# Optimization experiments

Hardware: AMD Instinct MI355X
Metric: run time of the kernel (lower is better)

## Reference

```python
import jax, jax.numpy as jnp
import numpy as np

N = 16384


def setup_inputs() -> dict:
    key = jax.random.key(0)
    k1, k2 = jax.random.split(key)
    logits = jax.random.normal(k1, (N,), dtype=jnp.float32)
    targets = jax.random.randint(k2, (N,), 0, 2, dtype=jnp.int64)
    return {"logits": logits, "targets": targets}


def reference(logits, targets):
    # sigmoid scores for every sample
    s = jax.nn.sigmoid(logits)  # [N]
    pos = (targets != 0).astype(s.dtype)  # [N] mask of positives
    neg = (targets == 0).astype(s.dtype)  # [N] mask of negatives
    # all-pairs pos-vs-neg surrogate: (1 - (s_pos - s_neg))^2
    d = 1.0 - (s[:, None] - s[None, :])  # [N, N]
    loss = jnp.sum((pos[:, None] * neg[None, :]) * (d * d))
    n_pos = jnp.sum(pos)
    n_neg = jnp.sum(neg)
    return loss / (n_pos * n_neg)
```

## Files before the change

### kernel.cpp

```cpp
#include <hip/hip_runtime.h>


#define BLOCK 1024

__global__ __launch_bounds__(BLOCK) void auc_stats_kernel(
    const float* __restrict__ logits, const int* __restrict__ targets,
    float* __restrict__ out, int n) {
  const int tid = threadIdx.x;

  float acc[6] = {0.f, 0.f, 0.f, 0.f, 0.f, 0.f};

  const int n4 = n >> 2;
  const float4* l4 = reinterpret_cast<const float4*>(logits);
  const int4*   t4 = reinterpret_cast<const int4*>(targets);

  for (int i = tid; i < n4; i += BLOCK) {
    float4 lv = l4[i];
    int4   tv = t4[i];
    float xs[4] = {lv.x, lv.y, lv.z, lv.w};
    int   ts[4] = {tv.x, tv.y, tv.z, tv.w};
#pragma unroll
    for (int k = 0; k < 4; ++k) {
      float s  = 1.0f / (1.0f + __expf(-xs[k]));
      float s2 = s * s;
      float p  = (ts[k] != 0) ? 1.0f : 0.0f;
      float q  = 1.0f - p;
      acc[0] += p;       acc[1] += q;
      acc[2] += p * s;   acc[3] += q * s;
      acc[4] += p * s2;  acc[5] += q * s2;
    }
  }
  for (int i = (n4 << 2) + tid; i < n; i += BLOCK) {
    float s  = 1.0f / (1.0f + __expf(-logits[i]));
    float s2 = s * s;
    float p  = (targets[i] != 0) ? 1.0f : 0.0f;
    float q  = 1.0f - p;
    acc[0] += p;       acc[1] += q;
    acc[2] += p * s;   acc[3] += q * s;
    acc[4] += p * s2;  acc[5] += q * s2;
  }

#pragma unroll
  for (int j = 0; j < 6; ++j) {
#pragma unroll
    for (int m = 1; m < 64; m <<= 1) {
      acc[j] += __shfl_xor(acc[j], m, 64);
    }
  }

  __shared__ float lds[BLOCK / 64][6];
  const int wave = tid >> 6;
  const int lane = tid & 63;
  if (lane == 0) {
#pragma unroll
    for (int j = 0; j < 6; ++j) lds[wave][j] = acc[j];
  }
  __syncthreads();

  if (tid == 0) {
    double t[6] = {0, 0, 0, 0, 0, 0};
    for (int w = 0; w < BLOCK / 64; ++w)
      for (int j = 0; j < 6; ++j) t[j] += (double)lds[w][j];

    double np_ = t[0], nn = t[1], sp = t[2], sn = t[3], sp2 = t[4], sn2 = t[5];
    double loss = np_ * nn
                - 2.0 * nn * sp
                + 2.0 * np_ * sn
                + nn * sp2
                + np_ * sn2
                - 2.0 * sp * sn;
    out[0] = (float)(loss / (np_ * nn));
  }
}

extern "C" void kernel_launch(void* const* d_in, const int* in_sizes, int n_in,
                              void* d_out, int out_size, void* d_ws, size_t ws_size,
                              hipStream_t stream) {
  const float* logits  = (const float*)d_in[0];
  const int*   targets = (const int*)d_in[1];
  float*       out     = (float*)d_out;
  const int n = in_sizes[0];

  auc_stats_kernel<<<dim3(1), dim3(BLOCK), 0, stream>>>(logits, targets, out, n);
}
```

Baseline: 10.77 us.

## Split reduction across 64 single-wave blocks with a second combine kernel

Replaces the single 1024-thread block with 64 blocks of one wave each, which write per-block partial sums to workspace. A second one-wave kernel reduces those partials in double and computes the final loss. This spreads the memory reads across many CUs instead of one, at the cost of an extra kernel launch and a global round trip.

```diff
diff --git a/kernel.cpp b/kernel.cpp
--- a/kernel.cpp
+++ b/kernel.cpp
@@ -1,12 +1,14 @@
 #include <hip/hip_runtime.h>
 
 
-#define BLOCK 1024
+#define G1 64
+#define B1 64
 
-__global__ __launch_bounds__(BLOCK) void auc_stats_kernel(
+__global__ __launch_bounds__(B1) void auc_partial_kernel(
     const float* __restrict__ logits, const int* __restrict__ targets,
-    float* __restrict__ out, int n) {
-  const int tid = threadIdx.x;
+    float* __restrict__ ws, int n) {
+  const int gtid = blockIdx.x * B1 + threadIdx.x;
+  const int nthreads = G1 * B1;
 
   float acc[6] = {0.f, 0.f, 0.f, 0.f, 0.f, 0.f};
 
@@ -14,7 +16,7 @@
   const float4* l4 = reinterpret_cast<const float4*>(logits);
   const int4*   t4 = reinterpret_cast<const int4*>(targets);
 
-  for (int i = tid; i < n4; i += BLOCK) {
+  for (int i = gtid; i < n4; i += nthreads) {
     float4 lv = l4[i];
     int4   tv = t4[i];
     float xs[4] = {lv.x, lv.y, lv.z, lv.w};
@@ -30,7 +32,7 @@
       acc[4] += p * s2;  acc[5] += q * s2;
     }
   }
-  for (int i = (n4 << 2) + tid; i < n; i += BLOCK) {
+  for (int i = (n4 << 2) + gtid; i < n; i += nthreads) {
     float s  = 1.0f / (1.0f + __expf(-logits[i]));
     float s2 = s * s;
     float p  = (targets[i] != 0) ? 1.0f : 0.0f;
@@ -48,20 +50,29 @@
     }
   }
 
-  __shared__ float lds[BLOCK / 64][6];
-  const int wave = tid >> 6;
-  const int lane = tid & 63;
+  if (threadIdx.x == 0) {
+#pragma unroll
+    for (int j = 0; j < 6; ++j) ws[blockIdx.x * 6 + j] = acc[j];
+  }
+}
+
+__global__ __launch_bounds__(64) void auc_combine_kernel(
+    const float* __restrict__ ws, float* __restrict__ out) {
+  const int lane = threadIdx.x;
+
+  double t[6];
+#pragma unroll
+  for (int j = 0; j < 6; ++j) t[j] = (double)ws[lane * 6 + j];
+
+#pragma unroll
+  for (int j = 0; j < 6; ++j) {
+#pragma unroll
+    for (int m = 1; m < 64; m <<= 1) {
+      t[j] += __shfl_xor(t[j], m, 64);
+    }
+  }
+
   if (lane == 0) {
-#pragma unroll
-    for (int j = 0; j < 6; ++j) lds[wave][j] = acc[j];
-  }
-  __syncthreads();
-
-  if (tid == 0) {
-    double t[6] = {0, 0, 0, 0, 0, 0};
-    for (int w = 0; w < BLOCK / 64; ++w)
-      for (int j = 0; j < 6; ++j) t[j] += (double)lds[w][j];
-
     double np_ = t[0], nn = t[1], sp = t[2], sn = t[3], sp2 = t[4], sn2 = t[5];
     double loss = np_ * nn
                 - 2.0 * nn * sp
@@ -79,7 +90,9 @@
   const float* logits  = (const float*)d_in[0];
   const int*   targets = (const int*)d_in[1];
   float*       out     = (float*)d_out;
+  float*       ws      = (float*)d_ws;
   const int n = in_sizes[0];
 
-  auc_stats_kernel<<<dim3(1), dim3(BLOCK), 0, stream>>>(logits, targets, out, n);
+  auc_partial_kernel<<<dim3(G1), dim3(B1), 0, stream>>>(logits, targets, ws, n);
+  auc_combine_kernel<<<dim3(1), dim3(64), 0, stream>>>(ws, out);
 }
```

Result: slower. 11.26 us (+4.6%).
